# Kernel tuning notes

Measured on AMD Instinct MI355X. Metric: run time of the kernel, lower is better.

The kernel has to match this reference:

```python
import jax, jax.numpy as jnp
import numpy as np

B, S = 1, 2048
HIDDEN = 4096
NQ, NKV, HD = 32, 8, 128
EPS = 1e-06
THETA = 10000.0


def setup_inputs() -> dict:
    key = jax.random.key(0)
    k0, k1, k2 = jax.random.split(key, 3)
    hidden_states = jax.random.normal(k0, (B, S, HIDDEN), jnp.float32)
    Wqkv = jax.random.normal(k1, (HIDDEN, (NQ + 2 * NKV) * HD), jnp.float32) * 0.02
    Wo = jax.random.normal(k2, (NQ * HD, HIDDEN), jnp.float32) * 0.02
    q_gamma = jnp.ones((HD,), jnp.float32)
    k_gamma = jnp.ones((HD,), jnp.float32)
    positions = jnp.broadcast_to(jnp.arange(S, dtype=jnp.int32), (B, S))
    # neox-style rotary tables: half head_dim frequencies
    inv_freq = 1.0 / (THETA ** (jnp.arange(0, HD, 2, dtype=jnp.float32) / HD))  # [HD/2]
    ang = positions[..., None].astype(jnp.float32) * inv_freq                   # [B,S,HD/2]
    return {
        'positions': positions,
        'hidden_states': hidden_states,
        'Wqkv': Wqkv,
        'Wo': Wo,
        'q_gamma': q_gamma,
        'k_gamma': k_gamma,
        'cos': jnp.cos(ang),
        'sin': jnp.sin(ang),
    }


def _rmsnorm(x, gamma):
    # per-head RMSNorm over last dim (head_dim)
    return x * jax.lax.rsqrt(jnp.mean(x * x, axis=-1, keepdims=True) + EPS) * gamma


def _rope(x, cos, sin):
    # x: [B,S,h,HD], cos/sin: [B,S,HD/2]; rotate-half (neox) style
    x1, x2 = jnp.split(x, 2, axis=-1)
    c = cos[:, :, None, :]
    s = sin[:, :, None, :]
    return jnp.concatenate([x1 * c - x2 * s, x2 * c + x1 * s], axis=-1)


def reference(positions, hidden_states, Wqkv, Wo, q_gamma, k_gamma, cos, sin):
    b, s, _ = hidden_states.shape
    qkv = hidden_states @ Wqkv                                  # [B,S,(NQ+2NKV)*HD]
    q, k, v = jnp.split(qkv, [NQ * HD, (NQ + NKV) * HD], axis=-1)
    q = _rmsnorm(q.reshape(b, s, NQ, HD), q_gamma)
    k = _rmsnorm(k.reshape(b, s, NKV, HD), k_gamma)
    v = v.reshape(b, s, NKV, HD)
    q = _rope(q, cos, sin)
    k = _rope(k, cos, sin)
    R = NQ // NKV                                               # GQA group size
    qg = q.reshape(b, s, NKV, R, HD)
    scores = jnp.einsum('bsgrd,btgd->bgrst', qg, k) * (HD ** -0.5)
    causal = jnp.tril(jnp.ones((s, s), bool))
    scores = jnp.where(causal, scores, jnp.finfo(scores.dtype).min)
    probs = jax.nn.softmax(scores, axis=-1)
    attn = jnp.einsum('bgrst,btgd->bsgrd', probs, v).reshape(b, s, NQ * HD)
    return attn @ Wo
```

## Files before the change

kernel.cpp:

```cpp
#include <hip/hip_runtime.h>
#include <hip/hip_bf16.h>


#define S_LEN   2048
#define HIDDEN  4096
#define NQ      32
#define NKV     8
#define HD      128
#define QKV_DIM 6144
#define NQHD    4096
#define K_OFF   4096
#define V_OFF   5120
#define EPSF    1e-6f

typedef _Float16 half8 __attribute__((ext_vector_type(8)));
typedef _Float16 half4v __attribute__((ext_vector_type(4)));
typedef _Float16 half2v __attribute__((ext_vector_type(2)));
typedef float floatx4 __attribute__((ext_vector_type(4)));

__device__ __forceinline__ void gload_lds16(const void* g, void* l) {
    __builtin_amdgcn_global_load_lds(
        (const __attribute__((address_space(1))) unsigned int*)g,
        (__attribute__((address_space(3))) unsigned int*)l, 16, 0, 0);
}

__global__ __launch_bounds__(256) void conv_f32_f16(const float* __restrict__ src,
                                                    _Float16* __restrict__ dst) {
    const size_t i = ((size_t)blockIdx.x * 256 + threadIdx.x) * 8;
    float4 a = *(const float4*)(src + i);
    float4 b = *(const float4*)(src + i + 4);
    half8 h;
    h[0] = (_Float16)a.x; h[1] = (_Float16)a.y; h[2] = (_Float16)a.z; h[3] = (_Float16)a.w;
    h[4] = (_Float16)b.x; h[5] = (_Float16)b.y; h[6] = (_Float16)b.z; h[7] = (_Float16)b.w;
    *(half8*)(dst + i) = h;
}

__global__ __launch_bounds__(256) void conv_w_transpose(const float* __restrict__ src,
                                                        _Float16* __restrict__ dst,
                                                        int N, int K) {
    __shared__ float T[64][65];
    const int tid = threadIdx.x;
    const int n0 = blockIdx.x * 64, k0 = blockIdx.y * 64;
    const int rr = tid >> 4, cc = (tid & 15) * 4;
    #pragma unroll
    for (int l = 0; l < 4; ++l) {
        const int r = rr + l * 16;
        *(float4*)&T[r][cc] = *(const float4*)(src + (size_t)(k0 + r) * N + n0 + cc);
    }
    __syncthreads();
    #pragma unroll
    for (int l = 0; l < 4; ++l) {
        const int rn = rr + l * 16;
        half4v h;
        h[0] = (_Float16)T[cc + 0][rn];
        h[1] = (_Float16)T[cc + 1][rn];
        h[2] = (_Float16)T[cc + 2][rn];
        h[3] = (_Float16)T[cc + 3][rn];
        *(half4v*)(dst + (size_t)(n0 + rn) * K + k0 + cc) = h;
    }
}

template <typename CT>
__global__ __launch_bounds__(256) void gemm_bt_f16(const _Float16* __restrict__ A,
                                                   const _Float16* __restrict__ Bt,
                                                   CT* __restrict__ C,
                                                   int K, int ldc) {
    __shared__ _Float16 As[128 * 32];
    __shared__ _Float16 Bs[128 * 32];

    const int tid = threadIdx.x;
    const int m0 = blockIdx.y * 128, n0 = blockIdx.x * 128;
    const int wave = tid >> 6, lane = tid & 63;
    const int fl = lane & 15, quad = lane >> 4;
    const int wm = (wave >> 1) * 64, wn = (wave & 1) * 64;

    const int srow = lane >> 2;
    const int skoff = (lane & 3) * 8;

    floatx4 acc[4][4] = {};

    for (int k0 = 0; k0 < K; k0 += 32) {
        __syncthreads();
        #pragma unroll
        for (int i = 0; i < 2; ++i) {
            const int chunk = wave * 2 + i;
            const int row = chunk * 16 + srow;
            gload_lds16(A + (size_t)(m0 + row) * K + k0 + skoff, &As[chunk * 512]);
            gload_lds16(Bt + (size_t)(n0 + row) * K + k0 + skoff, &Bs[chunk * 512]);
        }
        __syncthreads();

        half8 af[4], bf[4];
        #pragma unroll
        for (int t = 0; t < 4; ++t) {
            af[t] = *(const half8*)&As[(wm + t * 16 + fl) * 32 + quad * 8];
            bf[t] = *(const half8*)&Bs[(wn + t * 16 + fl) * 32 + quad * 8];
        }
        #pragma unroll
        for (int i = 0; i < 4; ++i)
            #pragma unroll
            for (int j = 0; j < 4; ++j)
                acc[i][j] = __builtin_amdgcn_mfma_f32_16x16x32_f16(
                    af[i], bf[j], acc[i][j], 0, 0, 0);
    }

    #pragma unroll
    for (int i = 0; i < 4; ++i)
        #pragma unroll
        for (int j = 0; j < 4; ++j)
            #pragma unroll
            for (int r = 0; r < 4; ++r)
                C[(size_t)(m0 + wm + i * 16 + quad * 4 + r) * ldc
                  + n0 + wn + j * 16 + fl] = (CT)acc[i][j][r];
}

__global__ __launch_bounds__(128) void rmsnorm_rope16(_Float16* __restrict__ qkv,
                                                      const float* __restrict__ qg,
                                                      const float* __restrict__ kg,
                                                      const float* __restrict__ cosb,
                                                      const float* __restrict__ sinb) {
    const int h = blockIdx.x;
    const int s = blockIdx.y;
    const int d = threadIdx.x;
    const bool isq = (h < NQ);
    const int off = isq ? h * HD : K_OFF + (h - NQ) * HD;
    _Float16* base = qkv + (size_t)s * QKV_DIM + off;

    float x = (float)base[d];
    float ss = x * x;
    #pragma unroll
    for (int o = 32; o; o >>= 1) ss += __shfl_xor(ss, o);

    __shared__ float red[2];
    __shared__ float sh[HD];
    if ((d & 63) == 0) red[d >> 6] = ss;
    __syncthreads();
    float tot = red[0] + red[1];
    float rms = rsqrtf(tot * (1.0f / (float)HD) + EPSF);
    const float* gamma = isq ? qg : kg;
    float xn = x * rms * gamma[d];
    sh[d] = xn;
    __syncthreads();

    float out;
    if (d < 64) {
        float c = cosb[s * 64 + d], sn = sinb[s * 64 + d];
        out = xn * c - sh[d + 64] * sn;
    } else {
        int j = d - 64;
        float c = cosb[s * 64 + j], sn = sinb[s * 64 + j];
        out = xn * c + sh[d - 64] * sn;
    }
    base[d] = (_Float16)out;
}

#define FAM 32
#define FAN 64
#define LQK 136
#define LVP 68

__global__ __launch_bounds__(256, 2) void flash_attn_gqa(
        const _Float16* __restrict__ qkv, _Float16* __restrict__ attn) {
    __shared__ __align__(16) _Float16 Ks[FAN][LQK];
    __shared__ __align__(16) _Float16 Vt[HD][LVP];
    __shared__ __align__(16) _Float16 Ps[4][FAM][LVP];

    const int tid = threadIdx.x;
    const int wave = tid >> 6, lane = tid & 63;
    const int fl = lane & 15, quad = lane >> 4;

    const int bd = blockIdx.x;
    const int c = bd & 255, sflip = bd >> 8;
    const int qt = sflip ? 63 - (c & 63) : (c & 63);
    const int kvh = (sflip << 2) + (c >> 6);
    const int h = kvh * 4 + wave;
    const int m0 = qt * FAM;
    const float scale = 0.08838834764831845f;

    half8 qf[2][4];
    #pragma unroll
    for (int mt = 0; mt < 2; ++mt)
        #pragma unroll
        for (int ks = 0; ks < 4; ++ks)
            qf[mt][ks] = *(const half8*)(qkv
                + (size_t)(m0 + mt * 16 + fl) * QKV_DIM + h * HD + ks * 32 + quad * 8);

    float m_prev[2][4], l_prev[2][4];
    #pragma unroll
    for (int mt = 0; mt < 2; ++mt)
        #pragma unroll
        for (int r = 0; r < 4; ++r) { m_prev[mt][r] = -1e30f; l_prev[mt][r] = 0.f; }
    floatx4 oacc[2][8] = {};

    const int tmax = (m0 + FAM - 1) / FAN;
    for (int t = 0; t <= tmax; ++t) {
        const int n0 = t * FAN;
        __syncthreads();

        #pragma unroll
        for (int l = 0; l < 4; ++l) {
            const int f = tid + l * 256;
            const int r = f >> 4, c8 = (f & 15) * 8;
            *(half8*)&Ks[r][c8] = *(const half8*)(qkv
                + (size_t)(n0 + r) * QKV_DIM + K_OFF + kvh * HD + c8);
        }
        {
            const int p = tid & 31, g0 = tid >> 5;
            #pragma unroll
            for (int gi = 0; gi < 2; ++gi) {
                const int g = g0 + gi * 8;
                const _Float16* v0p = qkv + (size_t)(n0 + 2 * p) * QKV_DIM
                                      + V_OFF + kvh * HD + 8 * g;
                half8 va = *(const half8*)v0p;
                half8 vb = *(const half8*)(v0p + QKV_DIM);
                #pragma unroll
                for (int i = 0; i < 8; ++i) {
                    half2v hh; hh[0] = va[i]; hh[1] = vb[i];
                    *(half2v*)&Vt[8 * g + i][2 * p] = hh;
                }
            }
        }
        __syncthreads();

        floatx4 sacc[2][4] = {};
        __builtin_amdgcn_s_setprio(1);
        #pragma unroll
        for (int ks = 0; ks < 4; ++ks)
            #pragma unroll
            for (int nt = 0; nt < 4; ++nt) {
                half8 bf = *(const half8*)&Ks[nt * 16 + fl][ks * 32 + quad * 8];
                sacc[0][nt] = __builtin_amdgcn_mfma_f32_16x16x32_f16(
                    qf[0][ks], bf, sacc[0][nt], 0, 0, 0);
                sacc[1][nt] = __builtin_amdgcn_mfma_f32_16x16x32_f16(
                    qf[1][ks], bf, sacc[1][nt], 0, 0, 0);
            }
        __builtin_amdgcn_s_setprio(0);

        const bool diag = (t == tmax);
        float mx[2][4];
        #pragma unroll
        for (int mt = 0; mt < 2; ++mt)
            #pragma unroll
            for (int r = 0; r < 4; ++r) mx[mt][r] = -1e30f;
        #pragma unroll
        for (int mt = 0; mt < 2; ++mt)
            #pragma unroll
            for (int nt = 0; nt < 4; ++nt)
                #pragma unroll
                for (int r = 0; r < 4; ++r) {
                    float sv = sacc[mt][nt][r] * scale;
                    if (diag && (n0 + nt * 16 + fl > m0 + mt * 16 + quad * 4 + r))
                        sv = -1e30f;
                    sacc[mt][nt][r] = sv;
                    mx[mt][r] = fmaxf(mx[mt][r], sv);
                }
        #pragma unroll
        for (int mt = 0; mt < 2; ++mt)
            #pragma unroll
            for (int r = 0; r < 4; ++r)
                #pragma unroll
                for (int o = 8; o; o >>= 1)
                    mx[mt][r] = fmaxf(mx[mt][r], __shfl_xor(mx[mt][r], o));

        float alpha[2][4], rs[2][4];
        #pragma unroll
        for (int mt = 0; mt < 2; ++mt)
            #pragma unroll
            for (int r = 0; r < 4; ++r) {
                float nm = fmaxf(m_prev[mt][r], mx[mt][r]);
                alpha[mt][r] = __expf(m_prev[mt][r] - nm);
                m_prev[mt][r] = nm;
                rs[mt][r] = 0.f;
            }
        #pragma unroll
        for (int mt = 0; mt < 2; ++mt)
            #pragma unroll
            for (int nt = 0; nt < 4; ++nt)
                #pragma unroll
                for (int r = 0; r < 4; ++r) {
                    float p = __expf(sacc[mt][nt][r] - m_prev[mt][r]);
                    rs[mt][r] += p;
                    Ps[wave][mt * 16 + quad * 4 + r][nt * 16 + fl] = (_Float16)p;
                }
        #pragma unroll
        for (int mt = 0; mt < 2; ++mt)
            #pragma unroll
            for (int r = 0; r < 4; ++r) {
                #pragma unroll
                for (int o = 8; o; o >>= 1) rs[mt][r] += __shfl_xor(rs[mt][r], o);
                l_prev[mt][r] = l_prev[mt][r] * alpha[mt][r] + rs[mt][r];
            }
        #pragma unroll
        for (int mt = 0; mt < 2; ++mt)
            #pragma unroll
            for (int dt = 0; dt < 8; ++dt)
                #pragma unroll
                for (int r = 0; r < 4; ++r) oacc[mt][dt][r] *= alpha[mt][r];

        __builtin_amdgcn_s_setprio(1);
        #pragma unroll
        for (int ks2 = 0; ks2 < 2; ++ks2) {
            half8 pa[2];
            #pragma unroll
            for (int mt = 0; mt < 2; ++mt) {
                half4v plo = *(const half4v*)&Ps[wave][mt * 16 + fl][ks2 * 32 + quad * 8];
                half4v phi = *(const half4v*)&Ps[wave][mt * 16 + fl][ks2 * 32 + quad * 8 + 4];
                pa[mt] = __builtin_shufflevector(plo, phi, 0, 1, 2, 3, 4, 5, 6, 7);
            }
            #pragma unroll
            for (int dt = 0; dt < 8; ++dt) {
                half4v vlo = *(const half4v*)&Vt[dt * 16 + fl][ks2 * 32 + quad * 8];
                half4v vhi = *(const half4v*)&Vt[dt * 16 + fl][ks2 * 32 + quad * 8 + 4];
                half8 vb = __builtin_shufflevector(vlo, vhi, 0, 1, 2, 3, 4, 5, 6, 7);
                oacc[0][dt] = __builtin_amdgcn_mfma_f32_16x16x32_f16(
                    pa[0], vb, oacc[0][dt], 0, 0, 0);
                oacc[1][dt] = __builtin_amdgcn_mfma_f32_16x16x32_f16(
                    pa[1], vb, oacc[1][dt], 0, 0, 0);
            }
        }
        __builtin_amdgcn_s_setprio(0);
    }

    #pragma unroll
    for (int mt = 0; mt < 2; ++mt) {
        float linv[4];
        #pragma unroll
        for (int r = 0; r < 4; ++r) linv[r] = 1.0f / l_prev[mt][r];
        #pragma unroll
        for (int dt = 0; dt < 8; ++dt)
            #pragma unroll
            for (int r = 0; r < 4; ++r)
                attn[(size_t)(m0 + mt * 16 + quad * 4 + r) * NQHD
                     + h * HD + dt * 16 + fl] = (_Float16)(oacc[mt][dt][r] * linv[r]);
    }
}

extern "C" void kernel_launch(void* const* d_in, const int* in_sizes, int n_in,
                              void* d_out, int out_size, void* d_ws, size_t ws_size,
                              hipStream_t stream) {
    const float* hidden = (const float*)d_in[1];
    const float* Wqkv   = (const float*)d_in[2];
    const float* Wo     = (const float*)d_in[3];
    const float* qg     = (const float*)d_in[4];
    const float* kg     = (const float*)d_in[5];
    const float* cosb   = (const float*)d_in[6];
    const float* sinb   = (const float*)d_in[7];
    float* out = (float*)d_out;

    _Float16* buf0  = (_Float16*)d_ws;
    _Float16* wT    = buf0 + (size_t)S_LEN * HIDDEN;
    _Float16* qkv16 = (_Float16*)d_out;
    _Float16* attn16 = buf0;

    conv_f32_f16<<<(S_LEN * HIDDEN) / 2048, 256, 0, stream>>>(hidden, buf0);
    conv_w_transpose<<<dim3(QKV_DIM / 64, HIDDEN / 64), 256, 0, stream>>>(
        Wqkv, wT, QKV_DIM, HIDDEN);
    gemm_bt_f16<_Float16><<<dim3(QKV_DIM / 128, S_LEN / 128), 256, 0, stream>>>(
        buf0, wT, qkv16, HIDDEN, QKV_DIM);
    rmsnorm_rope16<<<dim3(NQ + NKV, S_LEN), 128, 0, stream>>>(qkv16, qg, kg, cosb, sinb);
    flash_attn_gqa<<<dim3((S_LEN / FAM) * NKV), 256, 0, stream>>>(qkv16, attn16);
    conv_w_transpose<<<dim3(HIDDEN / 64, NQHD / 64), 256, 0, stream>>>(
        Wo, wT, HIDDEN, NQHD);
    gemm_bt_f16<float><<<dim3(HIDDEN / 128, S_LEN / 128), 256, 0, stream>>>(
        attn16, wT, out, NQHD, HIDDEN);
}
```

Before: 625.5 us.

## Rewrite FP16 GEMM with 256-wide tiles, double-buffered LDS and swizzled layout

Replaces the 128x128 single-buffered GEMM with a 512-thread kernel that uses 256xBM tiles and a K-step of 64. Global-to-LDS loads are double-buffered and prefetched two steps ahead, with explicit vmcnt waits, so memory traffic overlaps the MFMA work. LDS uses an XOR swizzle to avoid bank conflicts, workgroup IDs are remapped for cache locality, and MFMA sections raise wave priority. Larger tiles give more reuse but fewer blocks (48 and 64), so some CUs may sit idle, and the hand-coded vmcnt counts have to match the number of loads issued per stage.

```diff
diff --git a/kernel.cpp b/kernel.cpp
--- a/kernel.cpp
+++ b/kernel.cpp
@@ -60,58 +60,117 @@
     }
 }
 
-template <typename CT>
-__global__ __launch_bounds__(256) void gemm_bt_f16(const _Float16* __restrict__ A,
-                                                   const _Float16* __restrict__ Bt,
-                                                   CT* __restrict__ C,
-                                                   int K, int ldc) {
-    __shared__ _Float16 As[128 * 32];
-    __shared__ _Float16 Bs[128 * 32];
+template <typename CT, int BM>
+__global__ __launch_bounds__(512, 2) void gemm_bt_256(const _Float16* __restrict__ A,
+                                                      const _Float16* __restrict__ Bt,
+                                                      CT* __restrict__ C,
+                                                      int K, int ldc) {
+    constexpr int QM = BM / 128;
+    constexpr int AL = BM / 64;
+    constexpr int MI = QM * 4;
+
+    __shared__ _Float16 ldsA[2][BM * 64];
+    __shared__ _Float16 ldsB[2][256 * 64];
 
     const int tid = threadIdx.x;
-    const int m0 = blockIdx.y * 128, n0 = blockIdx.x * 128;
     const int wave = tid >> 6, lane = tid & 63;
     const int fl = lane & 15, quad = lane >> 4;
-    const int wm = (wave >> 1) * 64, wn = (wave & 1) * 64;
-
-    const int srow = lane >> 2;
-    const int skoff = (lane & 3) * 8;
-
-    floatx4 acc[4][4] = {};
-
-    for (int k0 = 0; k0 < K; k0 += 32) {
-        __syncthreads();
-        #pragma unroll
-        for (int i = 0; i < 2; ++i) {
-            const int chunk = wave * 2 + i;
-            const int row = chunk * 16 + srow;
-            gload_lds16(A + (size_t)(m0 + row) * K + k0 + skoff, &As[chunk * 512]);
-            gload_lds16(Bt + (size_t)(n0 + row) * K + k0 + skoff, &Bs[chunk * 512]);
-        }
-        __syncthreads();
-
-        half8 af[4], bf[4];
-        #pragma unroll
-        for (int t = 0; t < 4; ++t) {
-            af[t] = *(const half8*)&As[(wm + t * 16 + fl) * 32 + quad * 8];
-            bf[t] = *(const half8*)&Bs[(wn + t * 16 + fl) * 32 + quad * 8];
-        }
-        #pragma unroll
-        for (int i = 0; i < 4; ++i)
-            #pragma unroll
-            for (int j = 0; j < 4; ++j)
-                acc[i][j] = __builtin_amdgcn_mfma_f32_16x16x32_f16(
-                    af[i], bf[j], acc[i][j], 0, 0, 0);
-    }
-
-    #pragma unroll
-    for (int i = 0; i < 4; ++i)
-        #pragma unroll
-        for (int j = 0; j < 4; ++j)
+
+    const int nwg = gridDim.x * gridDim.y;
+    int bid = blockIdx.y * gridDim.x + blockIdx.x;
+    bid = (bid & 7) * (nwg >> 3) + (bid >> 3);
+    const int m0 = (bid / gridDim.x) * BM;
+    const int n0 = (bid % gridDim.x) * 256;
+
+    const int wm = (wave >> 2) * (BM / 2);
+    const int wn = (wave & 3) * 64;
+
+    const int srow8 = lane >> 3;
+    const int schunk = ((lane & 7) ^ srow8) * 8;
+
+    auto stage = [&](int p, int kt) {
+        const int kb = kt * 64;
+        #pragma unroll
+        for (int i = 0; i < AL; ++i) {
+            const int r0 = i * 64 + wave * 8;
+            gload_lds16(A + (size_t)(m0 + r0 + srow8) * K + kb + schunk,
+                        &ldsA[p][r0 * 64]);
+        }
+        #pragma unroll
+        for (int i = 0; i < 4; ++i) {
+            const int r0 = i * 64 + wave * 8;
+            gload_lds16(Bt + (size_t)(n0 + r0 + srow8) * K + kb + schunk,
+                        &ldsB[p][r0 * 64]);
+        }
+    };
+
+    floatx4 acc[MI][4] = {};
+
+    stage(0, 0);
+    stage(1, 1);
+
+    const int cs0 = ((quad ^ (fl & 7)) << 4);
+    const int cs1 = (((4 + quad) ^ (fl & 7)) << 4);
+
+    const int NT = K >> 6;
+    for (int t = 0; t < NT; ++t) {
+        if (t == NT - 1) {
+            asm volatile("s_waitcnt vmcnt(0)\n\ts_barrier" ::: "memory");
+        } else {
+            if constexpr (AL + 4 == 8)
+                asm volatile("s_waitcnt vmcnt(8)\n\ts_barrier" ::: "memory");
+            else
+                asm volatile("s_waitcnt vmcnt(6)\n\ts_barrier" ::: "memory");
+        }
+
+        const char* Asb = (const char*)ldsA[t & 1];
+        const char* Bsb = (const char*)ldsB[t & 1];
+
+        #pragma unroll
+        for (int qm = 0; qm < QM; ++qm) {
+            half8 af[4][2];
+            #pragma unroll
+            for (int mt = 0; mt < 4; ++mt) {
+                const char* rb = Asb + (wm + qm * 64 + mt * 16 + fl) * 128;
+                af[mt][0] = *(const half8*)(rb + cs0);
+                af[mt][1] = *(const half8*)(rb + cs1);
+            }
+            #pragma unroll
+            for (int qn = 0; qn < 2; ++qn) {
+                half8 bf[2][2];
+                #pragma unroll
+                for (int nt = 0; nt < 2; ++nt) {
+                    const char* rb = Bsb + (wn + qn * 32 + nt * 16 + fl) * 128;
+                    bf[nt][0] = *(const half8*)(rb + cs0);
+                    bf[nt][1] = *(const half8*)(rb + cs1);
+                }
+                __builtin_amdgcn_s_setprio(1);
+                #pragma unroll
+                for (int ks = 0; ks < 2; ++ks)
+                    #pragma unroll
+                    for (int mt = 0; mt < 4; ++mt)
+                        #pragma unroll
+                        for (int nt = 0; nt < 2; ++nt)
+                            acc[qm * 4 + mt][qn * 2 + nt] =
+                                __builtin_amdgcn_mfma_f32_16x16x32_f16(
+                                    af[mt][ks], bf[nt][ks],
+                                    acc[qm * 4 + mt][qn * 2 + nt], 0, 0, 0);
+                __builtin_amdgcn_s_setprio(0);
+            }
+        }
+
+        asm volatile("s_barrier" ::: "memory");
+        if (t + 2 < NT) stage(t & 1, t + 2);
+    }
+
+    #pragma unroll
+    for (int mi = 0; mi < MI; ++mi)
+        #pragma unroll
+        for (int ni = 0; ni < 4; ++ni)
             #pragma unroll
             for (int r = 0; r < 4; ++r)
-                C[(size_t)(m0 + wm + i * 16 + quad * 4 + r) * ldc
-                  + n0 + wn + j * 16 + fl] = (CT)acc[i][j][r];
+                C[(size_t)(m0 + wm + mi * 16 + quad * 4 + r) * ldc
+                  + n0 + wn + ni * 16 + fl] = (CT)acc[mi][ni][r];
 }
 
 __global__ __launch_bounds__(128) void rmsnorm_rope16(_Float16* __restrict__ qkv,
@@ -355,12 +414,12 @@
     conv_f32_f16<<<(S_LEN * HIDDEN) / 2048, 256, 0, stream>>>(hidden, buf0);
     conv_w_transpose<<<dim3(QKV_DIM / 64, HIDDEN / 64), 256, 0, stream>>>(
         Wqkv, wT, QKV_DIM, HIDDEN);
-    gemm_bt_f16<_Float16><<<dim3(QKV_DIM / 128, S_LEN / 128), 256, 0, stream>>>(
+    gemm_bt_256<_Float16, 256><<<dim3(QKV_DIM / 256, S_LEN / 256), 512, 0, stream>>>(
         buf0, wT, qkv16, HIDDEN, QKV_DIM);
     rmsnorm_rope16<<<dim3(NQ + NKV, S_LEN), 128, 0, stream>>>(qkv16, qg, kg, cosb, sinb);
     flash_attn_gqa<<<dim3((S_LEN / FAM) * NKV), 256, 0, stream>>>(qkv16, attn16);
     conv_w_transpose<<<dim3(HIDDEN / 64, NQHD / 64), 256, 0, stream>>>(
         Wo, wT, HIDDEN, NQHD);
-    gemm_bt_f16<float><<<dim3(HIDDEN / 128, S_LEN / 128), 256, 0, stream>>>(
+    gemm_bt_256<float, 128><<<dim3(HIDDEN / 256, S_LEN / 128), 512, 0, stream>>>(
         attn16, wT, out, NQHD, HIDDEN);
 }
```

Measured after the change: 605.0 us. 3.3% less time.

## Replace GEMM with 8-wave double-buffered pipelined kernel using swizzled LDS

Applied to the files above, without the earlier changes.

Replaces the simple single-buffered 128x128 GEMM with a 512-thread kernel using 256x256 and 256x128 tiles. It double-buffers LDS with async global-to-LDS loads issued between MFMA phases, uses fine-grained vmcnt waits and barriers, and raises MFMA priority with setprio. The kernel also XOR-swizzles LDS columns to avoid bank conflicts and remaps block IDs for cache locality. The aim is to hide memory latency and raise MFMA utilisation in both projection GEMMs, at the cost of hand-written synchronisation that relies on exact vmcnt counts and more registers per thread.

```diff
diff --git a/kernel.cpp b/kernel.cpp
--- a/kernel.cpp
+++ b/kernel.cpp
@@ -24,6 +24,23 @@
         (__attribute__((address_space(3))) unsigned int*)l, 16, 0, 0);
 }
 
+template <int N> __device__ __forceinline__ void vwait_bar() {
+    if constexpr (N == 0)
+        asm volatile("s_waitcnt vmcnt(0)\n\ts_barrier" ::: "memory");
+    else if constexpr (N == 3)
+        asm volatile("s_waitcnt vmcnt(3)\n\ts_barrier" ::: "memory");
+    else if constexpr (N == 4)
+        asm volatile("s_waitcnt vmcnt(4)\n\ts_barrier" ::: "memory");
+    else if constexpr (N == 6)
+        asm volatile("s_waitcnt vmcnt(6)\n\ts_barrier" ::: "memory");
+    else if constexpr (N == 8)
+        asm volatile("s_waitcnt vmcnt(8)\n\ts_barrier" ::: "memory");
+    else
+        asm volatile("s_waitcnt vmcnt(10)\n\ts_barrier" ::: "memory");
+}
+
+#define PHB asm volatile("s_barrier" ::: "memory")
+
 __global__ __launch_bounds__(256) void conv_f32_f16(const float* __restrict__ src,
                                                     _Float16* __restrict__ dst) {
     const size_t i = ((size_t)blockIdx.x * 256 + threadIdx.x) * 8;
@@ -60,59 +77,139 @@
     }
 }
 
-template <typename CT>
-__global__ __launch_bounds__(256) void gemm_bt_f16(const _Float16* __restrict__ A,
-                                                   const _Float16* __restrict__ Bt,
-                                                   CT* __restrict__ C,
-                                                   int K, int ldc) {
-    __shared__ _Float16 As[128 * 32];
-    __shared__ _Float16 Bs[128 * 32];
+#define MFMA_PH(NB)                                                            \
+    __builtin_amdgcn_s_setprio(1);                                             \
+    _Pragma("unroll")                                                          \
+    for (int mt = 0; mt < MI; ++mt)                                            \
+        _Pragma("unroll")                                                      \
+        for (int j = 0; j < NP; ++j)                                           \
+            acc[mt][(NB) + j] = __builtin_amdgcn_mfma_f32_16x16x32_f16(        \
+                af[mt], bf[j], acc[mt][(NB) + j], 0, 0, 0);                    \
+    __builtin_amdgcn_s_setprio(0);
+
+#define GEMM_TILE(KT, ST1, ST2, V1, V3)                                        \
+  {                                                                            \
+    const int cur_ = (KT) & 1;                                                 \
+    const char* bA0_ = (const char*)&sA[cur_][0][0] + rowA_ + csw;             \
+    const char* bA1_ = (const char*)&sA[cur_][1][0] + rowA_ + csw;             \
+    const char* bB0_ = (const char*)&sB[cur_][0][0] + rowB_ + csw;             \
+    const char* bB1_ = (const char*)&sB[cur_][1][0] + rowB_ + csw;             \
+    half8 af[MI]; half8 bf[NP];                                                \
+                                                 \
+    if (ST1) stageB(cur_ ^ 1, (KT) + 1, 1);                                    \
+    _Pragma("unroll") for (int mt = 0; mt < MI; ++mt)                          \
+        af[mt] = *(const half8*)(bA0_ + mt * 1024);                            \
+    _Pragma("unroll") for (int j = 0; j < NP; ++j)                             \
+        bf[j] = *(const half8*)(bB0_ + j * 1024);                              \
+    PHB;                                                                       \
+    MFMA_PH(0)                                                                 \
+    PHB;                                                                       \
+                                                 \
+    if (ST2) stageA(cur_, (KT) + 2, 0);                                        \
+    _Pragma("unroll") for (int j = 0; j < NP; ++j)                             \
+        bf[j] = *(const half8*)(bB0_ + (NP + j) * 1024);                       \
+    PHB;                                                                       \
+    MFMA_PH(NP)                                                                \
+    vwait_bar<V1>();                                                           \
+                                                 \
+    if (ST2) stageB(cur_, (KT) + 2, 0);                                        \
+    _Pragma("unroll") for (int mt = 0; mt < MI; ++mt)                          \
+        af[mt] = *(const half8*)(bA1_ + mt * 1024);                            \
+    _Pragma("unroll") for (int j = 0; j < NP; ++j)                             \
+        bf[j] = *(const half8*)(bB1_ + j * 1024);                              \
+    PHB;                                                                       \
+    MFMA_PH(0)                                                                 \
+    PHB;                                                                       \
+                                                 \
+    if (ST2) stageA(cur_, (KT) + 2, 1);                                        \
+    _Pragma("unroll") for (int j = 0; j < NP; ++j)                             \
+        bf[j] = *(const half8*)(bB1_ + (NP + j) * 1024);                       \
+    PHB;                                                                       \
+    MFMA_PH(NP)                                                                \
+    vwait_bar<V3>();                                                           \
+  }
+
+template <typename CT, int BM, int BN>
+__global__ __launch_bounds__(512, 2) void gemm_bt_8ph(const _Float16* __restrict__ A,
+                                                      const _Float16* __restrict__ Bt,
+                                                      CT* __restrict__ C,
+                                                      int K, int ldc) {
+    constexpr int AI = BM / 128;
+    constexpr int BI = BN / 128;
+    constexpr int MI = BM / 32;
+    constexpr int NI = BN / 64;
+    constexpr int NP = NI / 2;
+    constexpr int VNS = 3 * AI + 2 * BI;
+    constexpr int VT1 = 2 * AI + 2 * BI;
+    constexpr int VT3 = AI + BI;
+
+    __shared__ _Float16 sA[2][2][BM * 32];
+    __shared__ _Float16 sB[2][2][BN * 32];
 
     const int tid = threadIdx.x;
-    const int m0 = blockIdx.y * 128, n0 = blockIdx.x * 128;
     const int wave = tid >> 6, lane = tid & 63;
     const int fl = lane & 15, quad = lane >> 4;
-    const int wm = (wave >> 1) * 64, wn = (wave & 1) * 64;
-
-    const int srow = lane >> 2;
-    const int skoff = (lane & 3) * 8;
-
-    floatx4 acc[4][4] = {};
-
-    for (int k0 = 0; k0 < K; k0 += 32) {
-        __syncthreads();
-        #pragma unroll
-        for (int i = 0; i < 2; ++i) {
-            const int chunk = wave * 2 + i;
-            const int row = chunk * 16 + srow;
-            gload_lds16(A + (size_t)(m0 + row) * K + k0 + skoff, &As[chunk * 512]);
-            gload_lds16(Bt + (size_t)(n0 + row) * K + k0 + skoff, &Bs[chunk * 512]);
-        }
-        __syncthreads();
-
-        half8 af[4], bf[4];
-        #pragma unroll
-        for (int t = 0; t < 4; ++t) {
-            af[t] = *(const half8*)&As[(wm + t * 16 + fl) * 32 + quad * 8];
-            bf[t] = *(const half8*)&Bs[(wn + t * 16 + fl) * 32 + quad * 8];
-        }
-        #pragma unroll
-        for (int i = 0; i < 4; ++i)
-            #pragma unroll
-            for (int j = 0; j < 4; ++j)
-                acc[i][j] = __builtin_amdgcn_mfma_f32_16x16x32_f16(
-                    af[i], bf[j], acc[i][j], 0, 0, 0);
-    }
-
-    #pragma unroll
-    for (int i = 0; i < 4; ++i)
-        #pragma unroll
-        for (int j = 0; j < 4; ++j)
+    const int wm = (wave >> 2) * (BM / 2);
+    const int wn = (wave & 3) * (BN / 4);
+
+    const int nwg = gridDim.x * gridDim.y;
+    int bid = blockIdx.y * gridDim.x + blockIdx.x;
+    bid = (bid & 7) * (nwg >> 3) + (bid >> 3);
+    const int m0 = (bid / gridDim.x) * BM;
+    const int n0 = (bid % gridDim.x) * BN;
+
+    const int rl = lane >> 2;
+    const int gch = (((lane & 3) ^ (rl & 3) ^ ((rl >> 2) & 3))) * 8;
+    const int csw = ((quad ^ (fl & 3) ^ ((fl >> 2) & 3))) * 16;
+    const int rowA_ = (wm + fl) * 64;
+    const int rowB_ = (wn + fl) * 64;
+
+    auto stageA = [&](int buf, int T, int h) {
+        const _Float16* src = A + (size_t)(m0 + wave * 16 + rl) * K
+                              + T * 64 + h * 32 + gch;
+        _Float16* dst = &sA[buf][h][wave * 16 * 32];
+        #pragma unroll
+        for (int i = 0; i < AI; ++i)
+            gload_lds16(src + (size_t)(i * 128) * K, dst + i * 128 * 32);
+    };
+    auto stageB = [&](int buf, int T, int h) {
+        const _Float16* src = Bt + (size_t)(n0 + wave * 16 + rl) * K
+                              + T * 64 + h * 32 + gch;
+        _Float16* dst = &sB[buf][h][wave * 16 * 32];
+        #pragma unroll
+        for (int i = 0; i < BI; ++i)
+            gload_lds16(src + (size_t)(i * 128) * K, dst + i * 128 * 32);
+    };
+
+    floatx4 acc[MI][NI] = {};
+
+    stageA(0, 0, 0);
+    stageB(0, 0, 0);
+    stageA(0, 0, 1);
+    stageB(0, 0, 1);
+    stageA(1, 1, 0);
+    stageB(1, 1, 0);
+    stageA(1, 1, 1);
+    vwait_bar<VNS>();
+
+    const int NT = K >> 6;
+    for (int kt = 0; kt < NT - 2; ++kt)
+        GEMM_TILE(kt, true, true, VNS, VNS)
+    GEMM_TILE(NT - 2, true, false, VT1, VT3)
+    GEMM_TILE(NT - 1, false, false, 0, 0)
+
+    #pragma unroll
+    for (int mi = 0; mi < MI; ++mi)
+        #pragma unroll
+        for (int ni = 0; ni < NI; ++ni)
             #pragma unroll
             for (int r = 0; r < 4; ++r)
-                C[(size_t)(m0 + wm + i * 16 + quad * 4 + r) * ldc
-                  + n0 + wn + j * 16 + fl] = (CT)acc[i][j][r];
-}
+                C[(size_t)(m0 + wm + mi * 16 + quad * 4 + r) * ldc
+                  + n0 + wn + ni * 16 + fl] = (CT)acc[mi][ni][r];
+}
+
+#undef GEMM_TILE
+#undef MFMA_PH
 
 __global__ __launch_bounds__(128) void rmsnorm_rope16(_Float16* __restrict__ qkv,
                                                       const float* __restrict__ qg,
@@ -355,12 +452,12 @@
     conv_f32_f16<<<(S_LEN * HIDDEN) / 2048, 256, 0, stream>>>(hidden, buf0);
     conv_w_transpose<<<dim3(QKV_DIM / 64, HIDDEN / 64), 256, 0, stream>>>(
         Wqkv, wT, QKV_DIM, HIDDEN);
-    gemm_bt_f16<_Float16><<<dim3(QKV_DIM / 128, S_LEN / 128), 256, 0, stream>>>(
+    gemm_bt_8ph<_Float16, 256, 256><<<dim3(QKV_DIM / 256, S_LEN / 256), 512, 0, stream>>>(
         buf0, wT, qkv16, HIDDEN, QKV_DIM);
     rmsnorm_rope16<<<dim3(NQ + NKV, S_LEN), 128, 0, stream>>>(qkv16, qg, kg, cosb, sinb);
     flash_attn_gqa<<<dim3((S_LEN / FAM) * NKV), 256, 0, stream>>>(qkv16, attn16);
     conv_w_transpose<<<dim3(HIDDEN / 64, NQHD / 64), 256, 0, stream>>>(
         Wo, wT, HIDDEN, NQHD);
-    gemm_bt_f16<float><<<dim3(HIDDEN / 128, S_LEN / 128), 256, 0, stream>>>(
+    gemm_bt_8ph<float, 256, 128><<<dim3(HIDDEN / 128, S_LEN / 256), 512, 0, stream>>>(
         attn16, wT, out, NQHD, HIDDEN);
 }
```

Result: slower. 655.0 us (+4.7%).

## Double-buffer GEMM with swizzled LDS and widen rmsnorm-rope to one block per token

Applied to the files above, without the earlier changes.

The GEMM now uses a two-stage LDS ring with K-tile 64. The next tile's global-to-LDS loads are issued before computing on the current one, with vmcnt-based waits, an XOR swizzle against bank conflicts, and setprio around the MFMA bursts. The RMSNorm+RoPE kernel now runs one 256-thread block per token, with each wave handling whole heads through wave-level reductions, so the shared-memory barriers and the many tiny blocks go away. The GEMM doubles its LDS footprint to 64KB per block, which may limit occupancy, and the hand-written waitcnt logic depends on a precise count of outstanding loads.

```diff
diff --git a/kernel.cpp b/kernel.cpp
--- a/kernel.cpp
+++ b/kernel.cpp
@@ -61,47 +61,73 @@
 }
 
 template <typename CT>
-__global__ __launch_bounds__(256) void gemm_bt_f16(const _Float16* __restrict__ A,
-                                                   const _Float16* __restrict__ Bt,
-                                                   CT* __restrict__ C,
-                                                   int K, int ldc) {
-    __shared__ _Float16 As[128 * 32];
-    __shared__ _Float16 Bs[128 * 32];
+__global__ __launch_bounds__(256, 2) void gemm_bt_db(const _Float16* __restrict__ A,
+                                                     const _Float16* __restrict__ Bt,
+                                                     CT* __restrict__ C,
+                                                     int K, int ldc) {
+    __shared__ _Float16 sA[2][128 * 64];
+    __shared__ _Float16 sB[2][128 * 64];
 
     const int tid = threadIdx.x;
-    const int m0 = blockIdx.y * 128, n0 = blockIdx.x * 128;
     const int wave = tid >> 6, lane = tid & 63;
     const int fl = lane & 15, quad = lane >> 4;
+    const int m0 = blockIdx.y * 128, n0 = blockIdx.x * 128;
     const int wm = (wave >> 1) * 64, wn = (wave & 1) * 64;
 
-    const int srow = lane >> 2;
-    const int skoff = (lane & 3) * 8;
+    const int srow = lane >> 3;
+    const int sch  = ((lane & 7) ^ srow) * 8;
+
+    auto stage = [&](int p, int kt) {
+        const int kb = kt * 64;
+        #pragma unroll
+        for (int i = 0; i < 4; ++i) {
+            const int r0 = i * 32 + wave * 8;
+            gload_lds16(A + (size_t)(m0 + r0 + srow) * K + kb + sch,
+                        &sA[p][r0 * 64]);
+            gload_lds16(Bt + (size_t)(n0 + r0 + srow) * K + kb + sch,
+                        &sB[p][r0 * 64]);
+        }
+    };
 
     floatx4 acc[4][4] = {};
 
-    for (int k0 = 0; k0 < K; k0 += 32) {
-        __syncthreads();
-        #pragma unroll
-        for (int i = 0; i < 2; ++i) {
-            const int chunk = wave * 2 + i;
-            const int row = chunk * 16 + srow;
-            gload_lds16(A + (size_t)(m0 + row) * K + k0 + skoff, &As[chunk * 512]);
-            gload_lds16(Bt + (size_t)(n0 + row) * K + k0 + skoff, &Bs[chunk * 512]);
-        }
-        __syncthreads();
-
-        half8 af[4], bf[4];
-        #pragma unroll
-        for (int t = 0; t < 4; ++t) {
-            af[t] = *(const half8*)&As[(wm + t * 16 + fl) * 32 + quad * 8];
-            bf[t] = *(const half8*)&Bs[(wn + t * 16 + fl) * 32 + quad * 8];
-        }
-        #pragma unroll
-        for (int i = 0; i < 4; ++i)
-            #pragma unroll
-            for (int j = 0; j < 4; ++j)
-                acc[i][j] = __builtin_amdgcn_mfma_f32_16x16x32_f16(
-                    af[i], bf[j], acc[i][j], 0, 0, 0);
+    stage(0, 0);
+    stage(1, 1);
+
+    const int cs0 = (quad ^ (fl & 7)) << 4;
+    const int cs1 = ((4 + quad) ^ (fl & 7)) << 4;
+
+    const int NT = K >> 6;
+    for (int t = 0; t < NT; ++t) {
+        if (t == NT - 1)
+            asm volatile("s_waitcnt vmcnt(0)\n\ts_barrier" ::: "memory");
+        else
+            asm volatile("s_waitcnt vmcnt(8)\n\ts_barrier" ::: "memory");
+
+        const char* Ab = (const char*)&sA[t & 1][0];
+        const char* Bb = (const char*)&sB[t & 1][0];
+
+        #pragma unroll
+        for (int ks = 0; ks < 2; ++ks) {
+            const int cs = ks ? cs1 : cs0;
+            half8 af[4], bf[4];
+            #pragma unroll
+            for (int x = 0; x < 4; ++x) {
+                af[x] = *(const half8*)(Ab + (wm + x * 16 + fl) * 128 + cs);
+                bf[x] = *(const half8*)(Bb + (wn + x * 16 + fl) * 128 + cs);
+            }
+            __builtin_amdgcn_s_setprio(1);
+            #pragma unroll
+            for (int i = 0; i < 4; ++i)
+                #pragma unroll
+                for (int j = 0; j < 4; ++j)
+                    acc[i][j] = __builtin_amdgcn_mfma_f32_16x16x32_f16(
+                        af[i], bf[j], acc[i][j], 0, 0, 0);
+            __builtin_amdgcn_s_setprio(0);
+        }
+
+        asm volatile("s_barrier" ::: "memory");
+        if (t + 2 < NT) stage(t & 1, t + 2);
     }
 
     #pragma unroll
@@ -114,44 +140,34 @@
                   + n0 + wn + j * 16 + fl] = (CT)acc[i][j][r];
 }
 
-__global__ __launch_bounds__(128) void rmsnorm_rope16(_Float16* __restrict__ qkv,
+__global__ __launch_bounds__(256) void rmsnorm_rope_w(_Float16* __restrict__ qkv,
                                                       const float* __restrict__ qg,
                                                       const float* __restrict__ kg,
                                                       const float* __restrict__ cosb,
                                                       const float* __restrict__ sinb) {
-    const int h = blockIdx.x;
-    const int s = blockIdx.y;
-    const int d = threadIdx.x;
-    const bool isq = (h < NQ);
-    const int off = isq ? h * HD : K_OFF + (h - NQ) * HD;
-    _Float16* base = qkv + (size_t)s * QKV_DIM + off;
-
-    float x = (float)base[d];
-    float ss = x * x;
-    #pragma unroll
-    for (int o = 32; o; o >>= 1) ss += __shfl_xor(ss, o);
-
-    __shared__ float red[2];
-    __shared__ float sh[HD];
-    if ((d & 63) == 0) red[d >> 6] = ss;
-    __syncthreads();
-    float tot = red[0] + red[1];
-    float rms = rsqrtf(tot * (1.0f / (float)HD) + EPSF);
-    const float* gamma = isq ? qg : kg;
-    float xn = x * rms * gamma[d];
-    sh[d] = xn;
-    __syncthreads();
-
-    float out;
-    if (d < 64) {
-        float c = cosb[s * 64 + d], sn = sinb[s * 64 + d];
-        out = xn * c - sh[d + 64] * sn;
-    } else {
-        int j = d - 64;
-        float c = cosb[s * 64 + j], sn = sinb[s * 64 + j];
-        out = xn * c + sh[d - 64] * sn;
-    }
-    base[d] = (_Float16)out;
+    const int s = blockIdx.x;
+    const int wave = threadIdx.x >> 6, lane = threadIdx.x & 63;
+    const float c  = cosb[s * 64 + lane];
+    const float sn = sinb[s * 64 + lane];
+
+    #pragma unroll
+    for (int hi = 0; hi < 10; ++hi) {
+        const int h = hi * 4 + wave;
+        const bool isq = (h < NQ);
+        _Float16* base = qkv + (size_t)s * QKV_DIM
+                         + (isq ? h * HD : K_OFF + (h - NQ) * HD);
+        float x1 = (float)base[lane];
+        float x2 = (float)base[lane + 64];
+        float ss = x1 * x1 + x2 * x2;
+        #pragma unroll
+        for (int o = 32; o; o >>= 1) ss += __shfl_xor(ss, o);
+        float rms = rsqrtf(ss * (1.0f / (float)HD) + EPSF);
+        const float* g = isq ? qg : kg;
+        float xn1 = x1 * rms * g[lane];
+        float xn2 = x2 * rms * g[lane + 64];
+        base[lane]      = (_Float16)(xn1 * c - xn2 * sn);
+        base[lane + 64] = (_Float16)(xn2 * c + xn1 * sn);
+    }
 }
 
 #define FAM 32
@@ -355,12 +371,12 @@
     conv_f32_f16<<<(S_LEN * HIDDEN) / 2048, 256, 0, stream>>>(hidden, buf0);
     conv_w_transpose<<<dim3(QKV_DIM / 64, HIDDEN / 64), 256, 0, stream>>>(
         Wqkv, wT, QKV_DIM, HIDDEN);
-    gemm_bt_f16<_Float16><<<dim3(QKV_DIM / 128, S_LEN / 128), 256, 0, stream>>>(
+    gemm_bt_db<_Float16><<<dim3(QKV_DIM / 128, S_LEN / 128), 256, 0, stream>>>(
         buf0, wT, qkv16, HIDDEN, QKV_DIM);
-    rmsnorm_rope16<<<dim3(NQ + NKV, S_LEN), 128, 0, stream>>>(qkv16, qg, kg, cosb, sinb);
+    rmsnorm_rope_w<<<S_LEN, 256, 0, stream>>>(qkv16, qg, kg, cosb, sinb);
     flash_attn_gqa<<<dim3((S_LEN / FAM) * NKV), 256, 0, stream>>>(qkv16, attn16);
     conv_w_transpose<<<dim3(HIDDEN / 64, NQHD / 64), 256, 0, stream>>>(
         Wo, wT, HIDDEN, NQHD);
-    gemm_bt_f16<float><<<dim3(HIDDEN / 128, S_LEN / 128), 256, 0, stream>>>(
+    gemm_bt_db<float><<<dim3(HIDDEN / 128, S_LEN / 128), 256, 0, stream>>>(
         attn16, wT, out, NQHD, HIDDEN);
 }
```

After: 574.2 us. -8.2%, faster.
